# Optimization experiments

Hardware: AMD Instinct MI355X
Metric: run time of the kernel (lower is better)

The kernel has to match this reference:

```python
import jax, jax.numpy as jnp
import numpy as np

N, D, O, H, T, S, R, BN = 4096, 256, 256, 256, 512, 8, 4, 2  # nodes, in, out, hidden, text_len, adj_size, relations used, basis_num


def setup_inputs() -> dict:
    key = jax.random.key(0)
    ks = jax.random.split(key, 16)
    sc = 0.05
    return {
        "entity_embeddings": jax.random.normal(ks[0], (N, D), jnp.float32) * sc,
        "text_encodings": jax.random.normal(ks[1], (1, T, 2 * H), jnp.float32) * sc,
        "adj_to_use": jnp.arange(R, dtype=jnp.int32),
        "adj_masks": jax.random.randint(ks[2], (R, N, N), 0, 2, dtype=jnp.int32),
        "text_guids": jax.random.normal(ks[3], (S, 2 * H), jnp.float32) * sc,
        "graph_guids_1": jax.random.normal(ks[4], (S, D), jnp.float32) * sc,
        "graph_guids_2": jax.random.normal(ks[5], (S, D), jnp.float32) * sc,
        "guid_a": jax.random.normal(ks[6], (S,), jnp.float32),
        "basis_V": jax.random.normal(ks[7], (D, BN, O), jnp.float32) * sc,
        "basis_b": jax.random.normal(ks[8], (S, BN), jnp.float32) * sc,
        "W_1": jax.random.normal(ks[9], (2 * H, D), jnp.float32) * sc,
        "W_2": jax.random.normal(ks[10], (2 * H, D), jnp.float32) * sc,
        "ln_gamma": jnp.ones((O,), jnp.float32),
        "ln_beta": jnp.zeros((O,), jnp.float32),
    }


def reference(entity_embeddings, text_encodings, adj_to_use, adj_masks,
              text_guids, graph_guids_1, graph_guids_2, guid_a,
              basis_V, basis_b, W_1, W_2, ln_gamma, ln_beta):
    te = text_encodings[0]                                  # [T, 2H] (batch of 1)
    tg = text_guids[adj_to_use]                             # [R, 2H]
    # text attention: softmax over T, per relation
    att = jax.nn.softmax(te @ tg.T, axis=0)                 # [T, R]
    context = att.T @ te                                    # [R, 2H]
    c1 = context @ W_1                                      # [R, D]
    c2 = context @ W_2
    ga = jax.nn.sigmoid(guid_a[adj_to_use])[:, None]        # [R, 1]
    g1 = ga * graph_guids_1[adj_to_use] + (1.0 - ga) * c1   # [R, D]
    g2 = ga * graph_guids_2[adj_to_use] + (1.0 - ga) * c2
    s1 = entity_embeddings @ g1.T                           # [N, R]
    s2 = entity_embeddings @ g2.T
    # A[r,i,j] = s1[i,r] + s2[j,r], masked softmax over j
    A = s1.T[:, :, None] + s2.T[:, None, :]                 # [R, N, N]
    A = jnp.where(adj_masks == 1, A, jnp.float32(-1e10))
    A = jax.nn.softmax(A, axis=-1)
    fused = jnp.einsum('rij,jd->rid', A, entity_embeddings) # [R, N, D]
    # torch.cat over relations on last dim -> column index r*D + d
    fused_cat = jnp.transpose(fused, (1, 0, 2)).reshape(N, R * D)
    # torch.matmul([R,BN],[D,BN,O]) -> [D,R,O], then .view(R*D, O) (row index d*R + r)
    bb = basis_b[adj_to_use]                                # [R, BN]
    W = jnp.einsum('rb,dbo->dro', bb, basis_V).reshape(D * R, O)
    out = fused_cat @ W                                     # [N, O]
    mu = jnp.mean(out, axis=-1, keepdims=True)
    var = jnp.var(out, axis=-1, keepdims=True)
    out = (out - mu) / jnp.sqrt(var + 1e-5) * ln_gamma + ln_beta
    return jax.nn.relu(out)
```

## Files before the change

kernel.cpp:

```cpp
#include <hip/hip_runtime.h>
#include <hip/hip_bf16.h>


typedef unsigned short u16;
typedef short bf16x8 __attribute__((ext_vector_type(8)));
typedef float f32x4 __attribute__((ext_vector_type(4)));
typedef int   v4i   __attribute__((ext_vector_type(4)));
typedef unsigned int v2u __attribute__((ext_vector_type(2)));

#define G2_OFF    0
#define E2_OFF    4096
#define WRT_OFF   69632
#define FPT_OFF   593920
#define FUSED_OFF 9506816
#define CAN_OFF   26284032

#define C_ENT 0
#define C_TE  1048576
#define C_TG  1310720
#define C_GG2 1314816
#define C_GA  1316864
#define C_BV  1316872
#define C_BB  1447944
#define C_W2  1447960
#define C_GAM 1579032
#define C_BET 1579288

__device__ __forceinline__ float b2f(u16 u) {
    union { unsigned int i; float f; } v; v.i = ((unsigned int)u) << 16; return v.f;
}
__device__ __forceinline__ u16 f2b(float f) {
    union { float f; unsigned int i; } v; v.f = f;
    return (u16)((v.i + 0x7FFFu + ((v.i >> 16) & 1u)) >> 16);
}

__global__ __launch_bounds__(256) void k_cvt(
    const void* s0, const void* s1, const void* s2, const void* s3,
    const void* s4, const void* s5, const void* s6, const void* s7,
    const void* s8, const void* s9, const unsigned* __restrict__ graw,
    u16* __restrict__ dst)
{
    bool isbf = (graw[0] == 0x3F803F80u);
    const void* srcs[10] = {s0, s1, s2, s3, s4, s5, s6, s7, s8, s9};
    const int ns[10]     = {1048576, 262144, 4096, 2048, 8, 131072, 16, 131072, 256, 256};
    const int offs[10]   = {C_ENT, C_TE, C_TG, C_GG2, C_GA, C_BV, C_BB, C_W2, C_GAM, C_BET};
    const int bstart[11] = {0, 512, 640, 642, 643, 644, 708, 709, 773, 774, 775};
    int b = blockIdx.x, a = 0;
    while (b >= bstart[a + 1]) ++a;
    int rel = b - bstart[a];
    int n = ns[a];
    u16* d = dst + offs[a];
    int base = rel * 2048 + threadIdx.x;
    if (isbf) {
        const u16* s = (const u16*)srcs[a];
        for (int k = 0; k < 8; ++k) { int i = base + k * 256; if (i < n) d[i] = s[i]; }
    } else {
        const float* s = (const float*)srcs[a];
        for (int k = 0; k < 8; ++k) { int i = base + k * 256; if (i < n) d[i] = f2b(s[i]); }
    }
}

__global__ __launch_bounds__(1024) void k_pre(const u16* __restrict__ te,
                                              const int* __restrict__ adj,
                                              const u16* __restrict__ tguids,
                                              const u16* __restrict__ gg2,
                                              const u16* __restrict__ guida,
                                              const u16* __restrict__ W2,
                                              float* __restrict__ g2ws) {
    __shared__ float s_tg[4 * 512];
    __shared__ float s_att[512 * 4];
    __shared__ float s_red[512 * 4];
    __shared__ float s_ctx[4 * 512];
    __shared__ float s_part[1024 * 4];
    int tid = threadIdx.x;
    int a[4] = {adj[0], adj[1], adj[2], adj[3]};
    for (int idx = tid; idx < 2048; idx += 1024) {
        int r = idx >> 9, h = idx & 511;
        s_tg[r * 512 + h] = b2f(tguids[a[r] * 512 + h]);
    }
    __syncthreads();
    {
        int t = tid & 511, half = tid >> 9;
        int h0 = half * 256;
        float s0 = 0.f, s1 = 0.f, s2 = 0.f, s3 = 0.f;
        const u16* row = te + t * 512 + h0;
        for (int hb = 0; hb < 256; hb += 8) {
            bf16x8 v = *(const bf16x8*)(row + hb);
            #pragma unroll
            for (int k = 0; k < 8; ++k) {
                float tv = b2f((u16)v[k]);
                int h = h0 + hb + k;
                s0 += tv * s_tg[h];        s1 += tv * s_tg[512 + h];
                s2 += tv * s_tg[1024 + h]; s3 += tv * s_tg[1536 + h];
            }
        }
        s_part[tid * 4 + 0] = s0; s_part[tid * 4 + 1] = s1;
        s_part[tid * 4 + 2] = s2; s_part[tid * 4 + 3] = s3;
    }
    __syncthreads();
    if (tid < 512) {
        for (int r = 0; r < 4; ++r) {
            float s = s_part[tid * 4 + r] + s_part[(512 + tid) * 4 + r];
            s_att[tid * 4 + r] = s; s_red[tid * 4 + r] = s;
        }
    }
    __syncthreads();
    for (int st = 256; st > 0; st >>= 1) {
        if (tid < st) for (int r = 0; r < 4; ++r)
            s_red[tid * 4 + r] = fmaxf(s_red[tid * 4 + r], s_red[(tid + st) * 4 + r]);
        __syncthreads();
    }
    float mx[4]; for (int r = 0; r < 4; ++r) mx[r] = s_red[r];
    __syncthreads();
    if (tid < 512) for (int r = 0; r < 4; ++r) {
        float e = __expf(s_att[tid * 4 + r] - mx[r]);
        s_att[tid * 4 + r] = e; s_red[tid * 4 + r] = e;
    }
    __syncthreads();
    for (int st = 256; st > 0; st >>= 1) {
        if (tid < st) for (int r = 0; r < 4; ++r)
            s_red[tid * 4 + r] += s_red[(tid + st) * 4 + r];
        __syncthreads();
    }
    float dn[4]; for (int r = 0; r < 4; ++r) dn[r] = s_red[r];
    __syncthreads();
    if (tid < 512) for (int r = 0; r < 4; ++r) s_att[tid * 4 + r] /= dn[r];
    __syncthreads();
    {
        int u = tid >> 2, tq = tid & 3;
        int r = u >> 6, h0 = (u & 63) * 8;
        float acc[8] = {};
        int t0 = tq * 128;
        for (int t = t0; t < t0 + 128; ++t) {
            bf16x8 v = *(const bf16x8*)(te + t * 512 + h0);
            float at = s_att[t * 4 + r];
            #pragma unroll
            for (int k = 0; k < 8; ++k) acc[k] += at * b2f((u16)v[k]);
        }
        #pragma unroll
        for (int k = 0; k < 8; ++k) {
            acc[k] += __shfl_xor(acc[k], 1);
            acc[k] += __shfl_xor(acc[k], 2);
        }
        if (tq == 0) {
            #pragma unroll
            for (int k = 0; k < 8; ++k) s_ctx[r * 512 + h0 + k] = acc[k];
        }
    }
    __syncthreads();
    {
        int r = tid >> 8, d = tid & 255;
        float acc = 0.f;
        for (int h = 0; h < 512; ++h) acc += s_ctx[r * 512 + h] * b2f(W2[h * 256 + d]);
        float gav = 1.f / (1.f + expf(-b2f(guida[a[r]])));
        g2ws[r * 256 + d] = gav * b2f(gg2[a[r] * 256 + d]) + (1.f - gav) * acc;
    }
}

__global__ __launch_bounds__(256) void k_s2_wrt(const u16* __restrict__ entity,
                                                const int* __restrict__ adj,
                                                const u16* __restrict__ basisV,
                                                const u16* __restrict__ basisb,
                                                const float* __restrict__ g2ws,
                                                float* __restrict__ e2ws,
                                                u16* __restrict__ wrt) {
    int b = blockIdx.x, tid = threadIdx.x;
    if (b < 16) {
        __shared__ float sg2[1024];
        for (int i = tid; i < 1024; i += 256) sg2[i] = g2ws[i];
        __syncthreads();
        int j = b * 256 + tid;
        const u16* erow = entity + j * 256;
        float a0 = 0.f, a1 = 0.f, a2 = 0.f, a3 = 0.f;
        for (int d0 = 0; d0 < 256; d0 += 8) {
            bf16x8 v = *(const bf16x8*)(erow + d0);
            #pragma unroll
            for (int k = 0; k < 8; ++k) {
                float ev = b2f((u16)v[k]);
                a0 += ev * sg2[d0 + k];       a1 += ev * sg2[256 + d0 + k];
                a2 += ev * sg2[512 + d0 + k]; a3 += ev * sg2[768 + d0 + k];
            }
        }
        e2ws[j] = expf(a0); e2ws[4096 + j] = expf(a1);
        e2ws[8192 + j] = expf(a2); e2ws[12288 + j] = expf(a3);
    } else {
        int b2 = b - 16; int r = b2 >> 6;
        int c = (b2 & 63) * 4 + (tid >> 6);
        int dq = tid & 63;
        int dbase = dq * 4;
        int a[4] = {adj[0], adj[1], adj[2], adj[3]};
        for (int dd = 0; dd < 4; ++dd) {
            float w = 0.f;
            for (int bi = 0; bi < 2; ++bi)
                w += b2f(basisb[a[dd] * 2 + bi]) * b2f(basisV[((64 * r + dq) * 2 + bi) * 256 + c]);
            wrt[(r * 256 + c) * 256 + dbase + dd] = f2b(w);
        }
    }
}

__global__ __launch_bounds__(256) void k_fplus(const u16* __restrict__ entity,
                                               const u16* __restrict__ wrt,
                                               const float* __restrict__ e2ws,
                                               u16* __restrict__ fpt) {
    int b = blockIdx.x, tid = threadIdx.x;
    if (b < 256) {
        int r = b & 3, ct = (b >> 2) & 3, jt = b >> 4;
        int c0 = ct * 64, j0 = jt * 256;
        __shared__ __align__(16) u16 lw[64 * 264];
        const u16* wr = wrt + (r * 256 + c0) * 256;
        for (int k = 0; k < 8; ++k) {
            int ci = tid + k * 256; int row = ci >> 5, off = (ci & 31) * 8;
            *(v4i*)(&lw[row * 264 + off]) = *(const v4i*)(wr + row * 256 + off);
        }
        __syncthreads();
        int wave = tid >> 6, ln = tid & 15, q = (tid & 63) >> 4;
        f32x4 acc[4][4] = {};
        for (int ks = 0; ks < 8; ++ks) {
            bf16x8 afr[4], bfr[4];
            for (int mt = 0; mt < 4; ++mt)
                afr[mt] = *(const bf16x8*)(&lw[(mt * 16 + ln) * 264 + ks * 32 + q * 8]);
            for (int nt = 0; nt < 4; ++nt) {
                int j = j0 + (wave * 4 + nt) * 16 + ln;
                bfr[nt] = *(const bf16x8*)(entity + j * 256 + ks * 32 + q * 8);
            }
            for (int mt = 0; mt < 4; ++mt)
                for (int nt = 0; nt < 4; ++nt)
                    acc[mt][nt] = __builtin_amdgcn_mfma_f32_16x16x32_bf16(afr[mt], bfr[nt], acc[mt][nt], 0, 0, 0);
        }
        for (int nt = 0; nt < 4; ++nt) {
            int j = j0 + (wave * 4 + nt) * 16 + ln;
            float e2j = e2ws[r * 4096 + j];
            int kt = j >> 5, kk = j & 31;
            u16* dst = fpt + (((size_t)(r * 128 + kt)) * 272 << 5);
            for (int mt = 0; mt < 4; ++mt)
                for (int reg = 0; reg < 4; ++reg) {
                    int c = c0 + mt * 16 + q * 4 + reg;
                    dst[(c << 5) + kk] = f2b(acc[mt][nt][reg] * e2j);
                }
        }
    } else {
        int b2 = b - 256; int r = b2 >> 1, half = b2 & 1;
        const float* e2r = e2ws + r * 4096;
        for (int it = 0; it < 128; ++it) {
            int l = it * 256 + tid;
            int kk = l & 31;
            int c  = 256 + ((l >> 5) & 15);
            int kt = half * 64 + (l >> 9);
            fpt[(((size_t)(r * 128 + kt) * 272 + c) << 5) + kk] =
                (c == 256) ? f2b(e2r[kt * 32 + kk]) : (u16)0;
        }
    }
}

__global__ __launch_bounds__(512) void k_big(const int* __restrict__ masks,
                                             const u16* __restrict__ fpt,
                                             float* __restrict__ fused) {
    __shared__ __align__(16) u16 lm[64 * 40];
    __shared__ __align__(16) u16 lf[272 * 40];
    __shared__ float lden[64];
    int b = blockIdx.x, tid = threadIdx.x;
    int xcd = b & 7; int r = xcd & 3;
    int it = (b >> 3) + ((xcd >> 2) << 5);
    long i0 = (long)it * 64;
    const int* mbase = masks + ((long)r << 24) + i0 * 4096;
    const u16* fbase = fpt + (size_t)r * 128 * 272 * 32;
    int mrow = tid >> 3, mch = tid & 7;
    int wave = tid >> 6, lane = tid & 63, ln = lane & 15, q = lane >> 4;
    int mg = wave >> 2, ng = wave & 3;

    f32x4 acc[2][4] = {};
    f32x4 accD0 = {}, accD1 = {};

    struct Slot { v4i pm, p0, p1, p2; };
    Slot sA, sB, sC, sD;
    auto load_into = [&](int kt, Slot& s) {
        s.pm = __builtin_nontemporal_load((const v4i*)(mbase + mrow * 4096 + kt * 32 + mch * 4));
        const u16* su = fbase + (size_t)kt * 8704;
        s.p0 = *(const v4i*)(su + tid * 8);
        s.p1 = *(const v4i*)(su + (tid + 512) * 8);
        if (tid < 64) s.p2 = *(const v4i*)(su + (tid + 1024) * 8);
    };
    auto step = [&](int kt, Slot& s) {
        __syncthreads();
        {
            unsigned int m0 = (unsigned)s.pm.x * 0x3F80u, m1 = (unsigned)s.pm.y * 0x3F80u;
            unsigned int m2 = (unsigned)s.pm.z * 0x3F80u, m3 = (unsigned)s.pm.w * 0x3F80u;
            v2u w; w.x = m0 | (m1 << 16); w.y = m2 | (m3 << 16);
            *(v2u*)(&lm[mrow * 40 + mch * 4]) = w;
        }
        *(v4i*)(&lf[(tid >> 2) * 40 + (tid & 3) * 8]) = s.p0;
        { int ci = tid + 512; *(v4i*)(&lf[(ci >> 2) * 40 + (ci & 3) * 8]) = s.p1; }
        if (tid < 64) { int ci = tid + 1024; *(v4i*)(&lf[(ci >> 2) * 40 + (ci & 3) * 8]) = s.p2; }
        __syncthreads();
        if (kt + 4 < 128) load_into(kt + 4, s);
        bf16x8 a0 = *(const bf16x8*)(&lm[(mg * 32 + ln) * 40 + q * 8]);
        bf16x8 a1 = *(const bf16x8*)(&lm[(mg * 32 + 16 + ln) * 40 + q * 8]);
        #pragma unroll
        for (int nt = 0; nt < 4; ++nt) {
            bf16x8 bf = *(const bf16x8*)(&lf[((ng * 4 + nt) * 16 + ln) * 40 + q * 8]);
            acc[0][nt] = __builtin_amdgcn_mfma_f32_16x16x32_bf16(a0, bf, acc[0][nt], 0, 0, 0);
            acc[1][nt] = __builtin_amdgcn_mfma_f32_16x16x32_bf16(a1, bf, acc[1][nt], 0, 0, 0);
        }
        if (ng == 3) {
            bf16x8 bf = *(const bf16x8*)(&lf[(256 + ln) * 40 + q * 8]);
            accD0 = __builtin_amdgcn_mfma_f32_16x16x32_bf16(a0, bf, accD0, 0, 0, 0);
            accD1 = __builtin_amdgcn_mfma_f32_16x16x32_bf16(a1, bf, accD1, 0, 0, 0);
        }
    };

    load_into(0, sA);
    load_into(1, sB);
    load_into(2, sC);
    load_into(3, sD);
    #pragma unroll 1
    for (int kt = 0; kt < 128; kt += 4) {
        step(kt,     sA);
        step(kt + 1, sB);
        step(kt + 2, sC);
        step(kt + 3, sD);
    }

    if (ng == 3 && ln == 0) {
        #pragma unroll
        for (int reg = 0; reg < 4; ++reg) {
            lden[mg * 32 + q * 4 + reg]      = accD0[reg];
            lden[mg * 32 + 16 + q * 4 + reg] = accD1[reg];
        }
    }
    __syncthreads();
    float* fb = fused + ((long)r * 4096 + i0) * 256;
    #pragma unroll
    for (int mt = 0; mt < 2; ++mt) {
        float rd[4];
        #pragma unroll
        for (int reg = 0; reg < 4; ++reg) rd[reg] = 1.0f / lden[mg * 32 + mt * 16 + q * 4 + reg];
        #pragma unroll
        for (int nt = 0; nt < 4; ++nt) {
            int c = (ng * 4 + nt) * 16 + ln;
            #pragma unroll
            for (int reg = 0; reg < 4; ++reg) {
                int row = mg * 32 + mt * 16 + q * 4 + reg;
                __builtin_nontemporal_store(acc[mt][nt][reg] * rd[reg], fb + row * 256 + c);
            }
        }
    }
}

__global__ __launch_bounds__(256) void k_ln(const float* __restrict__ fused,
                                            const u16* __restrict__ gamma,
                                            const u16* __restrict__ beta,
                                            const unsigned* __restrict__ graw,
                                            void* __restrict__ outraw) {
    __shared__ float part[8];
    int i = blockIdx.x, o = threadIdx.x;
    float x = 0.f;
    for (int r = 0; r < 4; ++r)
        x += __builtin_nontemporal_load(fused + ((long)(r << 12) + i) * 256 + o);
    float s = x;
    #pragma unroll
    for (int st = 32; st > 0; st >>= 1) s += __shfl_xor(s, st);
    int w = o >> 6;
    if ((o & 63) == 0) part[w] = s;
    __syncthreads();
    float mu = (part[0] + part[1] + part[2] + part[3]) * (1.f / 256.f);
    float v = x - mu;
    float qv = v * v;
    #pragma unroll
    for (int st = 32; st > 0; st >>= 1) qv += __shfl_xor(qv, st);
    if ((o & 63) == 0) part[4 + w] = qv;
    __syncthreads();
    float var = (part[4] + part[5] + part[6] + part[7]) * (1.f / 256.f);
    float y = v * rsqrtf(var + 1e-5f) * b2f(gamma[o]) + b2f(beta[o]);
    float res = fmaxf(y, 0.f);
    bool isbf = (graw[0] == 0x3F803F80u);
    if (isbf) ((u16*)outraw)[i * 256 + o] = f2b(res);
    else      ((float*)outraw)[i * 256 + o] = res;
}

extern "C" void kernel_launch(void* const* d_in, const int* in_sizes, int n_in,
                              void* d_out, int out_size, void* d_ws, size_t ws_size,
                              hipStream_t stream) {
    const int* adj   = (const int*)d_in[2];
    const int* masks = (const int*)d_in[3];
    const unsigned* graw = (const unsigned*)d_in[12];
    char* ws = (char*)d_ws;
    float* g2ws = (float*)(ws + G2_OFF);
    float* e2ws = (float*)(ws + E2_OFF);
    u16*   wrt  = (u16*)(ws + WRT_OFF);
    u16*   fpt  = (u16*)(ws + FPT_OFF);
    float* fus  = (float*)(ws + FUSED_OFF);
    u16*   can  = (u16*)(ws + CAN_OFF);

    k_cvt<<<775, 256, 0, stream>>>(d_in[0], d_in[1], d_in[4], d_in[6], d_in[7],
                                   d_in[8], d_in[9], d_in[11], d_in[12], d_in[13],
                                   graw, can);
    const u16* entity = can + C_ENT;
    const u16* te     = can + C_TE;
    const u16* tguids = can + C_TG;
    const u16* gg2    = can + C_GG2;
    const u16* guida  = can + C_GA;
    const u16* basisV = can + C_BV;
    const u16* basisb = can + C_BB;
    const u16* W2     = can + C_W2;
    const u16* gamma  = can + C_GAM;
    const u16* beta   = can + C_BET;

    k_pre<<<1, 1024, 0, stream>>>(te, adj, tguids, gg2, guida, W2, g2ws);
    k_s2_wrt<<<272, 256, 0, stream>>>(entity, adj, basisV, basisb, g2ws, e2ws, wrt);
    k_fplus<<<264, 256, 0, stream>>>(entity, wrt, e2ws, fpt);
    k_big<<<256, 512, 0, stream>>>(masks, fpt, fus);
    k_ln<<<4096, 256, 0, stream>>>(fus, gamma, beta, graw, d_out);
}
```

Before: 552.5 us.

## Load mask fragments directly into registers and double-buffer feature tiles in LDS

The adjacency mask is now loaded by each lane straight into registers in the MFMA A-operand layout and converted to bf16 there, so it no longer passes through shared memory. The feature tile uses two LDS buffers: the next tile is staged while the current one is consumed, which cuts the loop to one barrier per step instead of two. In exchange, the four waves that share a row group each fetch the same mask rows from global memory, which raises cache and load traffic. The nontemporal hint on the mask load is dropped, and each slot holds more registers.

```diff
diff --git a/kernel.cpp b/kernel.cpp
--- a/kernel.cpp
+++ b/kernel.cpp
@@ -255,8 +255,7 @@
 __global__ __launch_bounds__(512) void k_big(const int* __restrict__ masks,
                                              const u16* __restrict__ fpt,
                                              float* __restrict__ fused) {
-    __shared__ __align__(16) u16 lm[64 * 40];
-    __shared__ __align__(16) u16 lf[272 * 40];
+    __shared__ __align__(16) u16 lf[2][272 * 40];
     __shared__ float lden[64];
     int b = blockIdx.x, tid = threadIdx.x;
     int xcd = b & 7; int r = xcd & 3;
@@ -264,60 +263,74 @@
     long i0 = (long)it * 64;
     const int* mbase = masks + ((long)r << 24) + i0 * 4096;
     const u16* fbase = fpt + (size_t)r * 128 * 272 * 32;
-    int mrow = tid >> 3, mch = tid & 7;
     int wave = tid >> 6, lane = tid & 63, ln = lane & 15, q = lane >> 4;
     int mg = wave >> 2, ng = wave & 3;
+    const int* mr0 = mbase + (mg * 32 + ln) * 4096 + q * 8;
+    const int* mr1 = mr0 + 16 * 4096;
 
     f32x4 acc[2][4] = {};
     f32x4 accD0 = {}, accD1 = {};
 
-    struct Slot { v4i pm, p0, p1, p2; };
-    Slot sA, sB, sC, sD;
-    auto load_into = [&](int kt, Slot& s) {
-        s.pm = __builtin_nontemporal_load((const v4i*)(mbase + mrow * 4096 + kt * 32 + mch * 4));
+    struct Slot { v4i f0, f1, f2, m00, m01, m10, m11; };
+    Slot s0, s1, s2, s3;
+    auto load_slot = [&](int kt, Slot& s) {
         const u16* su = fbase + (size_t)kt * 8704;
-        s.p0 = *(const v4i*)(su + tid * 8);
-        s.p1 = *(const v4i*)(su + (tid + 512) * 8);
-        if (tid < 64) s.p2 = *(const v4i*)(su + (tid + 1024) * 8);
+        s.f0 = *(const v4i*)(su + tid * 8);
+        s.f1 = *(const v4i*)(su + (tid + 512) * 8);
+        if (tid < 64) s.f2 = *(const v4i*)(su + (tid + 1024) * 8);
+        const int* p0 = mr0 + kt * 32;
+        const int* p1 = mr1 + kt * 32;
+        s.m00 = *(const v4i*)(p0);
+        s.m01 = *(const v4i*)(p0 + 4);
+        s.m10 = *(const v4i*)(p1);
+        s.m11 = *(const v4i*)(p1 + 4);
     };
-    auto step = [&](int kt, Slot& s) {
-        __syncthreads();
-        {
-            unsigned int m0 = (unsigned)s.pm.x * 0x3F80u, m1 = (unsigned)s.pm.y * 0x3F80u;
-            unsigned int m2 = (unsigned)s.pm.z * 0x3F80u, m3 = (unsigned)s.pm.w * 0x3F80u;
-            v2u w; w.x = m0 | (m1 << 16); w.y = m2 | (m3 << 16);
-            *(v2u*)(&lm[mrow * 40 + mch * 4]) = w;
-        }
-        *(v4i*)(&lf[(tid >> 2) * 40 + (tid & 3) * 8]) = s.p0;
-        { int ci = tid + 512; *(v4i*)(&lf[(ci >> 2) * 40 + (ci & 3) * 8]) = s.p1; }
-        if (tid < 64) { int ci = tid + 1024; *(v4i*)(&lf[(ci >> 2) * 40 + (ci & 3) * 8]) = s.p2; }
-        __syncthreads();
-        if (kt + 4 < 128) load_into(kt + 4, s);
-        bf16x8 a0 = *(const bf16x8*)(&lm[(mg * 32 + ln) * 40 + q * 8]);
-        bf16x8 a1 = *(const bf16x8*)(&lm[(mg * 32 + 16 + ln) * 40 + q * 8]);
+    auto cvt2 = [&](v4i lo, v4i hi) -> bf16x8 {
+        v4i w;
+        w.x = (int)((((unsigned)lo.x) | (((unsigned)lo.y) << 16)) * 0x3F80u);
+        w.y = (int)((((unsigned)lo.z) | (((unsigned)lo.w) << 16)) * 0x3F80u);
+        w.z = (int)((((unsigned)hi.x) | (((unsigned)hi.y) << 16)) * 0x3F80u);
+        w.w = (int)((((unsigned)hi.z) | (((unsigned)hi.w) << 16)) * 0x3F80u);
+        union { v4i i; bf16x8 h; } u; u.i = w; return u.h;
+    };
+    auto stage = [&](int par, const Slot& s) {
+        u16* dst = &lf[par][0];
+        *(v4i*)(dst + (tid >> 2) * 40 + (tid & 3) * 8) = s.f0;
+        { int ci = tid + 512; *(v4i*)(dst + (ci >> 2) * 40 + (ci & 3) * 8) = s.f1; }
+        if (tid < 64) { int ci = tid + 1024; *(v4i*)(dst + (ci >> 2) * 40 + (ci & 3) * 8) = s.f2; }
+    };
+    auto step = [&](int k, Slot& sM, Slot& sF) {
+        if (k + 1 < 128) stage((k + 1) & 1, sF);
+        bf16x8 a0 = cvt2(sM.m00, sM.m01);
+        bf16x8 a1 = cvt2(sM.m10, sM.m11);
+        if (k + 4 < 128) load_slot(k + 4, sM);
+        const u16* src = &lf[k & 1][0];
         #pragma unroll
         for (int nt = 0; nt < 4; ++nt) {
-            bf16x8 bf = *(const bf16x8*)(&lf[((ng * 4 + nt) * 16 + ln) * 40 + q * 8]);
+            bf16x8 bf = *(const bf16x8*)(src + ((ng * 4 + nt) * 16 + ln) * 40 + q * 8);
             acc[0][nt] = __builtin_amdgcn_mfma_f32_16x16x32_bf16(a0, bf, acc[0][nt], 0, 0, 0);
             acc[1][nt] = __builtin_amdgcn_mfma_f32_16x16x32_bf16(a1, bf, acc[1][nt], 0, 0, 0);
         }
         if (ng == 3) {
-            bf16x8 bf = *(const bf16x8*)(&lf[(256 + ln) * 40 + q * 8]);
+            bf16x8 bf = *(const bf16x8*)(src + (256 + ln) * 40 + q * 8);
             accD0 = __builtin_amdgcn_mfma_f32_16x16x32_bf16(a0, bf, accD0, 0, 0, 0);
             accD1 = __builtin_amdgcn_mfma_f32_16x16x32_bf16(a1, bf, accD1, 0, 0, 0);
         }
+        __syncthreads();
     };
 
-    load_into(0, sA);
-    load_into(1, sB);
-    load_into(2, sC);
-    load_into(3, sD);
+    load_slot(0, s0);
+    load_slot(1, s1);
+    load_slot(2, s2);
+    load_slot(3, s3);
+    stage(0, s0);
+    __syncthreads();
     #pragma unroll 1
     for (int kt = 0; kt < 128; kt += 4) {
-        step(kt,     sA);
-        step(kt + 1, sB);
-        step(kt + 2, sC);
-        step(kt + 3, sD);
+        step(kt,     s0, s1);
+        step(kt + 1, s1, s2);
+        step(kt + 2, s2, s3);
+        step(kt + 3, s3, s0);
     }
 
     if (ng == 3 && ln == 0) {
```

Measured after the change: 577.0 us. 1.04x slower.
